# Performance work log

Hardware: AMD Instinct MI355X
Metric: run time of the kernel (lower is better)

## Reference

```python
import jax, jax.numpy as jnp
import numpy as np

B, N, C, H = 16, 577, 768, 12
D = C // H
BETA = 1.0
KEEP_RATIO = 0.5


def setup_inputs() -> dict:
    key = jax.random.key(0)
    k0, k1, k2, k3 = jax.random.split(key, 4)
    x = jax.random.normal(k0, (B, N, C), dtype=jnp.float32)
    # UCB visit-count buffer, strictly positive as accumulated counts would be
    ucb_count_score = jax.random.uniform(k1, (H, N), dtype=jnp.float32) * 50.0 + 1.0
    Wqkv = jax.random.normal(k2, (3 * C, C), dtype=jnp.float32) * 0.02
    Wproj = jax.random.normal(k3, (C, C), dtype=jnp.float32) * 0.02
    bproj = jnp.zeros((C,), dtype=jnp.float32)
    counter = 60  # > 50 so pruning path is taken
    return {"x": x, "ucb_count_score": ucb_count_score, "Wqkv": Wqkv,
            "Wproj": Wproj, "bproj": bproj, "counter": counter}


def reference(x, ucb_count_score, Wqkv, Wproj, bproj, counter):
    # UCBAttention.forward with pruning_enabled=True, selection_mode='ucb',
    # ucb_update_enabled=True, exclude_cls=True, dropout=0 (eval).
    Bs, Ns, Cs = x.shape
    scale = D ** -0.5
    k_keep = max(1, int((Ns - 1) * KEEP_RATIO))  # _get_k with keep_ratio

    qkv = (x @ Wqkv.T).reshape(Bs, Ns, 3, H, D).transpose(2, 0, 3, 1, 4)  # [3,B,H,N,D]
    q, k, v = qkv[0], qkv[1], qkv[2]
    attn_scores = jnp.einsum('bhqd,bhkd->bhqk', q, k) * scale
    attn_probs = jax.nn.softmax(attn_scores, axis=-1)  # [B,H,N,N]

    # UCB scores over patches (CLS excluded)
    patch_scores = attn_probs[:, :, :, 1:].mean(axis=2)            # [B,H,N-1]
    expl = BETA * jnp.sqrt(jnp.log(counter + 1.0) / (ucb_count_score[:, 1:] + 1e-6))
    ucb_scores = patch_scores + expl[None, :, :]                   # [B,H,N-1]
    global_ucb = ucb_scores.mean(axis=1)                           # [B,N-1]
    _, topk_rel = jax.lax.top_k(global_ucb, k_keep)                # [B,k]
    kept = topk_rel + 1                                            # token indices

    # keep-vector: CLS (0) always kept; mask[i,j] = kept[i] OR kept[j]
    kv_mask = (jnp.zeros((Bs, Ns), attn_probs.dtype)
               .at[jnp.arange(Bs)[:, None], kept].set(1.0)
               .at[:, 0].set(1.0))                                 # [B,N]
    mask = jnp.maximum(kv_mask[:, None, :, None], kv_mask[:, None, None, :])  # [B,1,N,N]

    pruned = attn_probs * mask
    pruned = pruned / (pruned.sum(axis=-1, keepdims=True) + 1e-8)
    context = jnp.einsum('bhqk,bhkd->bhqd', pruned, v)             # [B,H,N,D]

    out = context.transpose(0, 2, 1, 3).reshape(Bs, Ns, Cs) @ Wproj.T + bproj

    # score_delta: +1/B at each kept token column, broadcast over heads
    delta = jnp.zeros((Ns,), jnp.float32).at[kept.reshape(-1)].add(1.0 / Bs)
    score_delta = jnp.broadcast_to(delta[None, :], ucb_count_score.shape)
    return out, score_delta, kept
```

## Files before the change

### kernel.cpp

```cpp
#include <hip/hip_runtime.h>
#include <cstdio>
#include <cstdint>

#define B_    16
#define N_    577
#define C_    768
#define H_    12
#define D_    64
#define KKEEP 288
#define SCALE 0.125f
#define LOG2E 1.4426950408889634f
#define M_TOT (B_ * N_)
#define NKT   24
#define PLROW ((size_t)N_ * 64)

typedef __bf16 bf16x8_t __attribute__((ext_vector_type(8)));
typedef __bf16 bf16x4_t __attribute__((ext_vector_type(4)));
typedef float  f32x4_t  __attribute__((ext_vector_type(4)));
typedef unsigned int u32x4_t __attribute__((ext_vector_type(4)));
typedef unsigned int u32x2_t __attribute__((ext_vector_type(2)));

__device__ __forceinline__ f32x4_t mfma_bf16(bf16x8_t a, bf16x8_t b, f32x4_t c) {
    return __builtin_amdgcn_mfma_f32_16x16x32_bf16(a, b, c, 0, 0, 0);
}

__device__ __forceinline__ void gload16(const ushort* g, ushort* l) {
    __builtin_amdgcn_global_load_lds(
        (const __attribute__((address_space(1))) void*)g,
        (__attribute__((address_space(3))) void*)l, 16, 0, 0);
}
#define VMCNT(n) asm volatile("s_waitcnt vmcnt(" #n ")" ::: "memory")
#define LGKM0()  asm volatile("s_waitcnt lgkmcnt(0)" ::: "memory")
#define SB() __builtin_amdgcn_sched_barrier(0)

__device__ __forceinline__ int xcd_swz(int bid, int nwg) {
    int q = nwg >> 3, r = nwg & 7;
    int xcd = bid & 7, off = bid >> 3;
    int base = (xcd < r) ? xcd * (q + 1) : r * (q + 1) + (xcd - r) * q;
    return base + off;
}

__device__ __forceinline__ void splitf(float x, unsigned int &hi, unsigned int &lo) {
    unsigned int u = __float_as_uint(x);
    hi = u >> 16;
    float r = x - __uint_as_float(u & 0xffff0000u);
    lo = __float_as_uint(r) >> 16;
}
__device__ __forceinline__ unsigned int bf16rne(float x) {
    unsigned int u = __float_as_uint(x);
    return (u + 0x7fffu + ((u >> 16) & 1u)) >> 16;
}

__device__ __forceinline__ void pack_tile(const float* __restrict__ src,
                                          ushort* __restrict__ dH,
                                          ushort* __restrict__ dL,
                                          int nrows, int tile) {
    int kt = tile % NKT, mt = tile / NKT;
    int w = threadIdx.x;
    int row = w >> 1, h = w & 1;
    int m = mt * 128 + row;
    int sw = (row >> 1) & 3;
    float f[16];
    if (m < nrows) {
        const float* s = src + (size_t)m * C_ + kt * 32;
        int sa = (2 * h) ^ sw, sb = (2 * h + 1) ^ sw;
        *(float4*)&f[0]  = *(const float4*)(s + sa * 8);
        *(float4*)&f[4]  = *(const float4*)(s + sa * 8 + 4);
        *(float4*)&f[8]  = *(const float4*)(s + sb * 8);
        *(float4*)&f[12] = *(const float4*)(s + sb * 8 + 4);
    } else {
#pragma unroll
        for (int i = 0; i < 16; i++) f[i] = 0.f;
    }
    unsigned hi[16], lo[16];
#pragma unroll
    for (int i = 0; i < 16; i++) splitf(f[i], hi[i], lo[i]);
    u32x4_t h0 = {hi[0] | (hi[1] << 16), hi[2] | (hi[3] << 16),
                  hi[4] | (hi[5] << 16), hi[6] | (hi[7] << 16)};
    u32x4_t h1 = {hi[8] | (hi[9] << 16), hi[10] | (hi[11] << 16),
                  hi[12] | (hi[13] << 16), hi[14] | (hi[15] << 16)};
    u32x4_t l0 = {lo[0] | (lo[1] << 16), lo[2] | (lo[3] << 16),
                  lo[4] | (lo[5] << 16), lo[6] | (lo[7] << 16)};
    u32x4_t l1 = {lo[8] | (lo[9] << 16), lo[10] | (lo[11] << 16),
                  lo[12] | (lo[13] << 16), lo[14] | (lo[15] << 16)};
    size_t dbase = (size_t)tile * 4096 + row * 32;
    *(u32x4_t*)&dH[dbase + (2 * h) * 8]     = h0;
    *(u32x4_t*)&dH[dbase + (2 * h + 1) * 8] = h1;
    *(u32x4_t*)&dL[dbase + (2 * h) * 8]     = l0;
    *(u32x4_t*)&dL[dbase + (2 * h + 1) * 8] = l1;
}

__device__ __forceinline__ void pack_tile_rne(const float* __restrict__ src,
                                              ushort* __restrict__ dst,
                                              int nrows, int tile) {
    int kt = tile % NKT, mt = tile / NKT;
    int w = threadIdx.x;
    int row = w >> 1, h = w & 1;
    int m = mt * 128 + row;
    int sw = (row >> 1) & 3;
    float f[16];
    if (m < nrows) {
        const float* s = src + (size_t)m * C_ + kt * 32;
        int sa = (2 * h) ^ sw, sb = (2 * h + 1) ^ sw;
        *(float4*)&f[0]  = *(const float4*)(s + sa * 8);
        *(float4*)&f[4]  = *(const float4*)(s + sa * 8 + 4);
        *(float4*)&f[8]  = *(const float4*)(s + sb * 8);
        *(float4*)&f[12] = *(const float4*)(s + sb * 8 + 4);
    } else {
#pragma unroll
        for (int i = 0; i < 16; i++) f[i] = 0.f;
    }
    unsigned hi[16];
#pragma unroll
    for (int i = 0; i < 16; i++) hi[i] = bf16rne(f[i]);
    u32x4_t h0 = {hi[0] | (hi[1] << 16), hi[2] | (hi[3] << 16),
                  hi[4] | (hi[5] << 16), hi[6] | (hi[7] << 16)};
    u32x4_t h1 = {hi[8] | (hi[9] << 16), hi[10] | (hi[11] << 16),
                  hi[12] | (hi[13] << 16), hi[14] | (hi[15] << 16)};
    size_t dbase = (size_t)tile * 4096 + row * 32;
    *(u32x4_t*)&dst[dbase + (2 * h) * 8]     = h0;
    *(u32x4_t*)&dst[dbase + (2 * h + 1) * 8] = h1;
}

#define NXP 1752
#define NWP 432
#define NPJ 144
#define NZ  37

__global__ __launch_bounds__(256) void pack_all_kernel(const float* __restrict__ x,
                                                       const float* __restrict__ Wqkv,
                                                       const float* __restrict__ Wproj,
                                                       ushort* __restrict__ XplH,
                                                       ushort* __restrict__ XplL,
                                                       ushort* __restrict__ WplH,
                                                       ushort* __restrict__ WplL,
                                                       ushort* __restrict__ Wpjb,
                                                       float* __restrict__ kvmask) {
    int bid = blockIdx.x;
    if (bid < NXP) {
        pack_tile(x, XplH, XplL, M_TOT, bid);
    } else if (bid < NXP + NWP) {
        pack_tile(Wqkv, WplH, WplL, 3 * C_, bid - NXP);
    } else if (bid < NXP + NWP + NPJ) {
        pack_tile_rne(Wproj, Wpjb, C_, bid - NXP - NWP);
    } else {
        int i = (bid - NXP - NWP - NPJ) * 256 + threadIdx.x;
        if (i < B_ * N_) kvmask[i] = 0.f;
    }
}

__device__ __forceinline__ bf16x8_t fragT(const ushort* H, int row, int c, int ls) {
    int phys = ((c << 2) + ls) ^ (row & 7);
    return __builtin_bit_cast(bf16x8_t, *(const u32x4_t*)&H[(row << 6) + (phys << 3)]);
}

__global__ __launch_bounds__(256) void gemm_qkv_mfma(const ushort* __restrict__ XplH,
                                                     const ushort* __restrict__ XplL,
                                                     const ushort* __restrict__ WplH,
                                                     const ushort* __restrict__ WplL,
                                                     ushort* __restrict__ qhp,
                                                     ushort* __restrict__ qlp,
                                                     ushort* __restrict__ khp,
                                                     ushort* __restrict__ klp,
                                                     ushort* __restrict__ vtp) {
    __shared__ ushort SMEM[24576];
    ushort* Ah = SMEM;
    ushort* Al = SMEM + 8192;
    ushort* Bh = SMEM + 16384;
    ushort* Bl = SMEM + 20480;
    const int bid = xcd_swz(blockIdx.x, 18 * 73);
    const int bx = bid % 18, by = bid / 18;
    const int tid = threadIdx.x;
    const int lane = tid & 63, wave = tid >> 6;
    const int wr = wave >> 1, wc = wave & 1;
    const int lr = lane & 15, ls = lane >> 4;
    const int m0 = by * 128;
    const int o0 = wave * 1024, o1 = o0 + 512;
    const int la = lane * 8;
    const size_t abase = (size_t)by * NKT * 4096;
    const size_t bbase = (size_t)bx * NKT * 4096;
    f32x4_t acc[4][4] = {};

    if (bx < 12) {
        auto stageA = [&](int buf, int kt) {
            const size_t ta = abase + (size_t)kt * 4096;
            gload16(XplH + ta + o0 + la, &Ah[buf * 4096 + o0]);
            gload16(XplH + ta + o1 + la, &Ah[buf * 4096 + o1]);
            gload16(XplL + ta + o0 + la, &Al[buf * 4096 + o0]);
            gload16(XplL + ta + o1 + la, &Al[buf * 4096 + o1]);
        };
        auto stageB = [&](int kt) {
            const size_t tb = bbase + (size_t)kt * 4096;
            gload16(WplH + tb + o0 + la, &Bh[o0]);
            gload16(WplH + tb + o1 + la, &Bh[o1]);
            gload16(WplL + tb + o0 + la, &Bl[o0]);
            gload16(WplL + tb + o1 + la, &Bl[o1]);
        };
        stageA(0, 0);
        stageB(0);
        VMCNT(0);
        SB(); __builtin_amdgcn_s_barrier(); SB();
#pragma unroll 1
        for (int kt = 0; kt < NKT; ++kt) {
            const int cur = kt & 1;
            if (kt + 1 < NKT) stageA(cur ^ 1, kt + 1);
            bf16x8_t fah[4], fal[4], fbh[4], fbl[4];
#pragma unroll
            for (int i = 0; i < 4; i++) {
                int rowA = wr * 64 + i * 16 + lr;
                int pa = ls ^ ((rowA >> 1) & 3);
                fah[i] = __builtin_bit_cast(bf16x8_t, *(const u32x4_t*)&Ah[cur * 4096 + rowA * 32 + pa * 8]);
                fal[i] = __builtin_bit_cast(bf16x8_t, *(const u32x4_t*)&Al[cur * 4096 + rowA * 32 + pa * 8]);
                int rowB = wc * 64 + i * 16 + lr;
                int pb = ls ^ ((rowB >> 1) & 3);
                fbh[i] = __builtin_bit_cast(bf16x8_t, *(const u32x4_t*)&Bh[rowB * 32 + pb * 8]);
                fbl[i] = __builtin_bit_cast(bf16x8_t, *(const u32x4_t*)&Bl[rowB * 32 + pb * 8]);
            }
            LGKM0(); SB();
            __builtin_amdgcn_s_barrier();
            SB();
            if (kt + 1 < NKT) stageB(kt + 1);
            __builtin_amdgcn_s_setprio(1);
#pragma unroll
            for (int i = 0; i < 4; i++)
#pragma unroll
                for (int j = 0; j < 4; j++) {
                    acc[i][j] = mfma_bf16(fah[i], fbh[j], acc[i][j]);
                    acc[i][j] = mfma_bf16(fah[i], fbl[j], acc[i][j]);
                    acc[i][j] = mfma_bf16(fal[i], fbh[j], acc[i][j]);
                }
            __builtin_amdgcn_s_setprio(0);
            if (kt + 1 < NKT) {
                VMCNT(0); SB();
                __builtin_amdgcn_s_barrier();
                SB();
            }
        }
        const int n0 = bx * 128;
        const int s = n0 / C_;
        __syncthreads();
        unsigned* T = (unsigned*)SMEM;
        const float sc = (s == 0) ? SCALE * LOG2E : 1.0f;
        ushort* dh = (s == 1) ? khp : qhp;
        ushort* dl = (s == 1) ? klp : qlp;
        const int hh0 = (n0 % C_) / D_;
#pragma unroll 1
        for (int round = 0; round < 2; ++round) {
            if (wr == round) {
#pragma unroll
                for (int j = 0; j < 4; j++) {
                    int nl = wc * 64 + j * 16 + lr;
#pragma unroll
                    for (int i = 0; i < 4; i++) {
#pragma unroll
                        for (int r = 0; r < 4; r++) {
                            int ml = wr * 64 + i * 16 + ls * 4 + r;
                            unsigned hi, lo;
                            splitf(acc[i][j][r] * sc, hi, lo);
                            int idx = (ml & 63) * 128 +
                                      ((((nl >> 3) ^ ((ml >> 2) & 7)) << 3) | (nl & 7));
                            T[idx] = hi | (lo << 16);
                        }
                    }
                }
            }
            __syncthreads();
#pragma unroll
            for (int it = 0; it < 4; ++it) {
                int g = it * 256 + tid;
                int sl = g & 7;
                int m_local64 = (g >> 3) & 63;
                int hh_half = g >> 9;
                int m_local = round * 64 + m_local64;
                int m = m0 + m_local;
                if (m < M_TOT) {
                    int b = m / N_, n = m % N_;
                    int dg = sl ^ (n & 7);
                    int grp = (hh_half * 8 + dg) ^ ((m_local >> 2) & 7);
                    const unsigned* src = &T[m_local64 * 128 + grp * 8];
                    u32x4_t a = *(const u32x4_t*)src;
                    u32x4_t bvv = *(const u32x4_t*)(src + 4);
                    u32x4_t hiv = {(a[0] & 0xffffu) | (a[1] << 16),
                                   (a[2] & 0xffffu) | (a[3] << 16),
                                   (bvv[0] & 0xffffu) | (bvv[1] << 16),
                                   (bvv[2] & 0xffffu) | (bvv[3] << 16)};
                    u32x4_t lov = {(a[0] >> 16) | (a[1] & 0xffff0000u),
                                   (a[2] >> 16) | (a[3] & 0xffff0000u),
                                   (bvv[0] >> 16) | (bvv[1] & 0xffff0000u),
                                   (bvv[2] >> 16) | (bvv[3] & 0xffff0000u)};
                    size_t off = (size_t)(b * H_ + hh0 + hh_half) * PLROW + (size_t)n * 64 + sl * 8;
                    *(u32x4_t*)&dh[off] = hiv;
                    *(u32x4_t*)&dl[off] = lov;
                }
            }
            if (round == 0) __syncthreads();
        }
    } else {
        auto stageA = [&](int buf, int kt) {
            const size_t ta = abase + (size_t)kt * 4096;
            gload16(XplH + ta + o0 + la, &Ah[buf * 4096 + o0]);
            gload16(XplH + ta + o1 + la, &Ah[buf * 4096 + o1]);
            gload16(XplL + ta + o0 + la, &Al[buf * 4096 + o0]);
            gload16(XplL + ta + o1 + la, &Al[buf * 4096 + o1]);
        };
        auto stageB = [&](int kt) {
            const size_t tb = bbase + (size_t)kt * 4096;
            gload16(WplH + tb + o0 + la, &Bh[o0]);
            gload16(WplH + tb + o1 + la, &Bh[o1]);
        };
        stageA(0, 0);
        stageB(0);
        VMCNT(0);
        SB(); __builtin_amdgcn_s_barrier(); SB();
#pragma unroll 1
        for (int kt = 0; kt < NKT; ++kt) {
            const int cur = kt & 1;
            if (kt + 1 < NKT) stageA(cur ^ 1, kt + 1);
            bf16x8_t fah[4], fal[4], fbh[4];
#pragma unroll
            for (int i = 0; i < 4; i++) {
                int rowA = wr * 64 + i * 16 + lr;
                int pa = ls ^ ((rowA >> 1) & 3);
                fah[i] = __builtin_bit_cast(bf16x8_t, *(const u32x4_t*)&Ah[cur * 4096 + rowA * 32 + pa * 8]);
                fal[i] = __builtin_bit_cast(bf16x8_t, *(const u32x4_t*)&Al[cur * 4096 + rowA * 32 + pa * 8]);
                int rowB = wc * 64 + i * 16 + lr;
                int pb = ls ^ ((rowB >> 1) & 3);
                fbh[i] = __builtin_bit_cast(bf16x8_t, *(const u32x4_t*)&Bh[rowB * 32 + pb * 8]);
            }
            LGKM0(); SB();
            __builtin_amdgcn_s_barrier();
            SB();
            if (kt + 1 < NKT) stageB(kt + 1);
            __builtin_amdgcn_s_setprio(1);
#pragma unroll
            for (int i = 0; i < 4; i++)
#pragma unroll
                for (int j = 0; j < 4; j++) {
                    acc[i][j] = mfma_bf16(fah[i], fbh[j], acc[i][j]);
                    acc[i][j] = mfma_bf16(fal[i], fbh[j], acc[i][j]);
                }
            __builtin_amdgcn_s_setprio(0);
            if (kt + 1 < NKT) {
                VMCNT(0); SB();
                __builtin_amdgcn_s_barrier();
                SB();
            }
        }
        const int n0v = (bx - 12) * 128;
#pragma unroll
        for (int j = 0; j < 4; j++) {
            int ng = n0v + wc * 64 + j * 16 + lr;
            int hh = ng / D_;
            int d = ng % D_;
#pragma unroll
            for (int i = 0; i < 4; i++) {
                int mg0 = m0 + wr * 64 + i * 16 + ls * 4;
#pragma unroll
                for (int r = 0; r < 4; r++) {
                    int m = mg0 + r;
                    if (m < M_TOT) {
                        int b = m / N_, n = m % N_;
                        int jt = n >> 6, jl = n & 63;
                        size_t off = ((size_t)(b * H_ + hh) * 10 + jt) * 4096 +
                                     (size_t)d * 64 + (((jl >> 3) ^ (d & 7)) << 3) + (jl & 7);
                        vtp[off] = __builtin_bit_cast(unsigned short, (__bf16)acc[i][j][r]);
                    }
                }
            }
        }
    }
}

__global__ __launch_bounds__(512) void attn_rowsum_mfma(const ushort* __restrict__ qh,
                                                        const ushort* __restrict__ ql,
                                                        const ushort* __restrict__ kh,
                                                        const ushort* __restrict__ kl,
                                                        float* __restrict__ w) {
    __shared__ ushort Qh[8192], Ql[8192];
    __shared__ ushort Kh[4096], Kl[4096];
    __shared__ float red[8][64];
    const int bid = xcd_swz(blockIdx.x, 5 * B_ * H_);
    const int bh = bid / 5, q0 = (bid % 5) * 128;
    const int tid = threadIdx.x, lane = tid & 63, wv = tid >> 6;
    const int wg = wv >> 2, wl = wv & 3;
    const int lr = lane & 15, ls = lane >> 4;
    const size_t bho = (size_t)bh * PLROW;
    const ushort* qhp = qh + bho; const ushort* qlp = ql + bho;
    const ushort* khp = kh + bho; const ushort* klp = kl + bho;
    auto qrow = [&](int rr) { return (size_t)min(q0 + wv * 16 + rr * 8 + (lane >> 3), N_ - 1) * 64 + (lane & 7) * 8; };
    gload16(qhp + qrow(0), &Qh[wv * 1024]);
    gload16(qhp + qrow(1), &Qh[wv * 1024 + 512]);
    gload16(qlp + qrow(0), &Ql[wv * 1024]);
    gload16(qlp + qrow(1), &Ql[wv * 1024 + 512]);
    auto krow = [&](int j0) { return (size_t)min(j0 + wv * 8 + (lane >> 3), N_ - 1) * 64 + (lane & 7) * 8; };
    auto stageK = [&](int j0) {
        gload16(khp + krow(j0), &Kh[wv * 512]);
        gload16(klp + krow(j0), &Kl[wv * 512]);
    };
    stageK(0);
    VMCNT(0);
    __syncthreads();
    bf16x8_t fqh[4][2], fql[4][2];
#pragma unroll
    for (int i = 0; i < 4; i++)
#pragma unroll
        for (int c = 0; c < 2; c++) {
            fqh[i][c] = fragT(Qh, wg * 64 + i * 16 + lr, c, ls);
            fql[i][c] = fragT(Ql, wg * 64 + i * 16 + lr, c, ls);
        }
    float rs[4] = {0.f, 0.f, 0.f, 0.f};
#pragma unroll 1
    for (int t = 0; t < 10; ++t) {
        bf16x8_t fkh[2], fkl[2];
#pragma unroll
        for (int c = 0; c < 2; c++) {
            fkh[c] = fragT(Kh, wl * 16 + lr, c, ls);
            fkl[c] = fragT(Kl, wl * 16 + lr, c, ls);
        }
        LGKM0(); SB();
        __builtin_amdgcn_s_barrier();
        SB();
        if (t < 9) stageK((t + 1) * 64);
        int jbase = t * 64 + wl * 16 + ls * 4;
#pragma unroll
        for (int i = 0; i < 4; i++) {
            f32x4_t s = {0.f, 0.f, 0.f, 0.f};
            __builtin_amdgcn_s_setprio(1);
#pragma unroll
            for (int c = 0; c < 2; c++) {
                s = mfma_bf16(fkh[c], fqh[i][c], s);
                s = mfma_bf16(fkh[c], fql[i][c], s);
                s = mfma_bf16(fkl[c], fqh[i][c], s);
            }
            __builtin_amdgcn_s_setprio(0);
#pragma unroll
            for (int r = 0; r < 4; r++)
                rs[i] += (jbase + r < N_) ? __builtin_amdgcn_exp2f(s[r]) : 0.f;
        }
        if (t < 9) {
            VMCNT(0); SB();
            __builtin_amdgcn_s_barrier();
            SB();
        }
    }
#pragma unroll
    for (int i = 0; i < 4; i++) {
        float v2 = rs[i];
        v2 += __shfl_xor(v2, 16);
        v2 += __shfl_xor(v2, 32);
        if (ls == 0) red[wv][i * 16 + lr] = v2;
    }
    __syncthreads();
    if (tid < 128) {
        int grp = tid >> 6, qlc = tid & 63;
        float s = red[grp * 4 + 0][qlc] + red[grp * 4 + 1][qlc] +
                  red[grp * 4 + 2][qlc] + red[grp * 4 + 3][qlc];
        int qn = q0 + tid;
        if (qn < N_) w[(size_t)bh * N_ + qn] = 1.0f / s;
    }
}

__global__ __launch_bounds__(512) void attn_colsum_mfma(const ushort* __restrict__ qh,
                                                        const ushort* __restrict__ ql,
                                                        const ushort* __restrict__ kh,
                                                        const ushort* __restrict__ kl,
                                                        const float* __restrict__ w,
                                                        float* __restrict__ colsum) {
    __shared__ ushort KhS[8192], KlS[8192];
    __shared__ ushort Qh[4096], Ql[4096];
    __shared__ float wsAll[640];
    __shared__ float red[8][64];
    const int bid = xcd_swz(blockIdx.x, 5 * B_ * H_);
    const int bh = bid / 5, j0 = (bid % 5) * 128;
    const int tid = threadIdx.x, lane = tid & 63, wv = tid >> 6;
    const int wg = wv >> 2, wl = wv & 3;
    const int lr = lane & 15, ls = lane >> 4;
    const size_t bho = (size_t)bh * PLROW;
    const ushort* qhp = qh + bho; const ushort* qlp = ql + bho;
    const ushort* khp = kh + bho; const ushort* klp = kl + bho;
    auto krow = [&](int rr) { return (size_t)min(j0 + wv * 16 + rr * 8 + (lane >> 3), N_ - 1) * 64 + (lane & 7) * 8; };
    gload16(khp + krow(0), &KhS[wv * 1024]);
    gload16(khp + krow(1), &KhS[wv * 1024 + 512]);
    gload16(klp + krow(0), &KlS[wv * 1024]);
    gload16(klp + krow(1), &KlS[wv * 1024 + 512]);
    auto qrow2 = [&](int qt) { return (size_t)min(qt + wv * 8 + (lane >> 3), N_ - 1) * 64 + (lane & 7) * 8; };
    auto stageQ = [&](int qt) {
        gload16(qhp + qrow2(qt), &Qh[wv * 512]);
        gload16(qlp + qrow2(qt), &Ql[wv * 512]);
    };
    stageQ(0);
    for (int i2 = tid; i2 < 640; i2 += 512)
        wsAll[i2] = (i2 < N_) ? w[(size_t)bh * N_ + i2] : 0.f;
    VMCNT(0);
    __syncthreads();
    bf16x8_t fkh[4][2], fkl[4][2];
#pragma unroll
    for (int i = 0; i < 4; i++)
#pragma unroll
        for (int c = 0; c < 2; c++) {
            fkh[i][c] = fragT(KhS, wg * 64 + i * 16 + lr, c, ls);
            fkl[i][c] = fragT(KlS, wg * 64 + i * 16 + lr, c, ls);
        }
    float cs[4] = {0.f, 0.f, 0.f, 0.f};
#pragma unroll 1
    for (int t = 0; t < 10; ++t) {
        bf16x8_t fqh[2], fql[2];
#pragma unroll
        for (int c = 0; c < 2; c++) {
            fqh[c] = fragT(Qh, wl * 16 + lr, c, ls);
            fql[c] = fragT(Ql, wl * 16 + lr, c, ls);
        }
        float wq[4];
#pragma unroll
        for (int r = 0; r < 4; r++) wq[r] = wsAll[t * 64 + wl * 16 + ls * 4 + r];
        LGKM0(); SB();
        __builtin_amdgcn_s_barrier();
        SB();
        if (t < 9) stageQ((t + 1) * 64);
#pragma unroll
        for (int i = 0; i < 4; i++) {
            f32x4_t s = {0.f, 0.f, 0.f, 0.f};
            __builtin_amdgcn_s_setprio(1);
#pragma unroll
            for (int c = 0; c < 2; c++) {
                s = mfma_bf16(fqh[c], fkh[i][c], s);
                s = mfma_bf16(fql[c], fkh[i][c], s);
                s = mfma_bf16(fqh[c], fkl[i][c], s);
            }
            __builtin_amdgcn_s_setprio(0);
#pragma unroll
            for (int r = 0; r < 4; r++) cs[i] += __builtin_amdgcn_exp2f(s[r]) * wq[r];
        }
        if (t < 9) {
            VMCNT(0); SB();
            __builtin_amdgcn_s_barrier();
            SB();
        }
    }
#pragma unroll
    for (int i = 0; i < 4; i++) {
        float v2 = cs[i];
        v2 += __shfl_xor(v2, 16);
        v2 += __shfl_xor(v2, 32);
        if (ls == 0) red[wv][i * 16 + lr] = v2;
    }
    __syncthreads();
    if (tid < 128) {
        int grp = tid >> 6, jlc = tid & 63;
        float t2 = red[grp * 4 + 0][jlc] + red[grp * 4 + 1][jlc] +
                   red[grp * 4 + 2][jlc] + red[grp * 4 + 3][jlc];
        int jn = j0 + tid;
        if (jn < N_) colsum[(size_t)bh * N_ + jn] = t2;
    }
}

__global__ __launch_bounds__(512) void topk_kernel(const float* __restrict__ colsum,
                                                   const float* __restrict__ ucb_count,
                                                   const int* __restrict__ counter,
                                                   float* __restrict__ kept_out,
                                                   float* __restrict__ kvmask) {
    __shared__ float sv[1024];
    __shared__ int si[1024];
    int b = blockIdx.x, tid = threadIdx.x;
    float lc = logf((float)counter[0] + 1.0f);
    for (int t = tid; t < 1024; t += 512) {
        if (t < N_ - 1) {
            int tok = t + 1;
            float accv = 0.f;
#pragma unroll
            for (int h = 0; h < H_; h++) {
                float csv = colsum[(size_t)(b * H_ + h) * N_ + tok];
                float patch = csv * (1.0f / (float)N_);
                float cnt = ucb_count[h * N_ + tok];
                float expl = sqrtf(lc / (cnt + 1e-6f));
                accv += patch + expl;
            }
            sv[t] = accv * (1.0f / (float)H_);
            si[t] = t;
        } else {
            sv[t] = -INFINITY;
            si[t] = 1 << 20;
        }
    }
    __syncthreads();
    for (int kk = 2; kk <= 1024; kk <<= 1) {
        for (int jj = kk >> 1; jj > 0; jj >>= 1) {
            for (int t = tid; t < 1024; t += 512) {
                int ixj = t ^ jj;
                if (ixj > t) {
                    float v1 = sv[t], v2 = sv[ixj];
                    int i1 = si[t], i2 = si[ixj];
                    bool before21 = (v2 > v1) || (v2 == v1 && i2 < i1);
                    bool dirDesc = ((t & kk) == 0);
                    if (before21 == dirDesc) {
                        sv[t] = v2; sv[ixj] = v1;
                        si[t] = i2; si[ixj] = i1;
                    }
                }
            }
            __syncthreads();
        }
    }
    for (int r = tid; r < KKEEP; r += 512) {
        int tok = si[r] + 1;
        kept_out[b * KKEEP + r] = (float)tok;
        kvmask[b * N_ + tok] = 1.0f;
    }
    if (tid == 0) kvmask[b * N_] = 1.0f;
}

__global__ __launch_bounds__(512) void attn_ctx_mfma(const ushort* __restrict__ qh,
                                                     const ushort* __restrict__ ql,
                                                     const ushort* __restrict__ kh,
                                                     const ushort* __restrict__ vtp,
                                                     const float* __restrict__ kvmask,
                                                     ushort* __restrict__ ctxb,
                                                     float* __restrict__ sd) {
    if (blockIdx.x >= 5 * B_ * H_) {
        int idx = (blockIdx.x - 5 * B_ * H_) * 512 + threadIdx.x;
        if (idx < H_ * N_) {
            int n = idx % N_;
            float d = 0.f;
            if (n != 0) {
#pragma unroll
                for (int b = 0; b < B_; b++) d += kvmask[b * N_ + n];
            }
            sd[idx] = d * (1.0f / (float)B_);
        }
        return;
    }
    __shared__ ushort Kh[4096], Vt[4096];
    __shared__ ushort Pl[2][4096];
    __shared__ float mkAll[640];
    float (*red)[64] = (float(*)[64])&Pl[0][0];
    float* inv = (float*)&Pl[1][0];
    const int bid = xcd_swz(blockIdx.x, 5 * B_ * H_);
    const int bh = bid / 5, q0 = (bid % 5) * 128;
    const int b = bh / H_, h = bh % H_;
    const int tid = threadIdx.x, lane = tid & 63, wv = tid >> 6;
    const int wg = wv >> 2, wl = wv & 3;
    const int lr = lane & 15, ls = lane >> 4;
    const size_t bho = (size_t)bh * PLROW;
    const ushort* qhp = qh + bho; const ushort* qlp = ql + bho;
    const ushort* khp = kh + bho;
    const ushort* vtb = vtp + (size_t)bh * 10 * 4096;
    ushort* PlS = &Pl[0][0];
    for (int i2 = tid; i2 < 640; i2 += 512)
        mkAll[i2] = (i2 < N_) ? kvmask[(size_t)b * N_ + i2] : 0.f;
    auto qrow = [&](int rr) { return (size_t)min(q0 + wv * 16 + rr * 8 + (lane >> 3), N_ - 1) * 64 + (lane & 7) * 8; };
    bf16x8_t fqh[4][2], fql[4][2];
    gload16(qhp + qrow(0), &PlS[wv * 1024]);
    gload16(qhp + qrow(1), &PlS[wv * 1024 + 512]);
    VMCNT(0); __syncthreads();
#pragma unroll
    for (int i = 0; i < 4; i++)
#pragma unroll
        for (int c = 0; c < 2; c++)
            fqh[i][c] = fragT(PlS, wg * 64 + i * 16 + lr, c, ls);
    __syncthreads();
    gload16(qlp + qrow(0), &PlS[wv * 1024]);
    gload16(qlp + qrow(1), &PlS[wv * 1024 + 512]);
    VMCNT(0); __syncthreads();
#pragma unroll
    for (int i = 0; i < 4; i++)
#pragma unroll
        for (int c = 0; c < 2; c++)
            fql[i][c] = fragT(PlS, wg * 64 + i * 16 + lr, c, ls);
    __syncthreads();
    auto krow = [&](int j0) { return (size_t)min(j0 + wv * 8 + (lane >> 3), N_ - 1) * 64 + (lane & 7) * 8; };
    auto stageKV = [&](int t) {
        gload16(khp + krow(t * 64), &Kh[wv * 512]);
        gload16(vtb + (size_t)t * 4096 + wv * 512 + lane * 8, &Vt[wv * 512]);
    };
    float mq[4];
#pragma unroll
    for (int i = 0; i < 4; i++) mq[i] = mkAll[q0 + wg * 64 + i * 16 + lr];
    stageKV(0);
    VMCNT(0);
    SB(); __builtin_amdgcn_s_barrier(); SB();
    f32x4_t acc[4] = {};
    float psums[4] = {0.f, 0.f, 0.f, 0.f};
#pragma unroll 1
    for (int t = 0; t < 10; ++t) {
        bf16x8_t fkh[2], fv[2];
#pragma unroll
        for (int c = 0; c < 2; c++) {
            fkh[c] = fragT(Kh, wl * 16 + lr, c, ls);
            fv[c]  = fragT(Vt, wl * 16 + lr, c, ls);
        }
        LGKM0(); SB();
        __builtin_amdgcn_s_barrier();
        SB();
        if (t < 9) stageKV(t + 1);
        int jloc = wl * 16 + ls * 4;
        float jmv[4], jbias[4];
#pragma unroll
        for (int r = 0; r < 4; r++) {
            int j = t * 64 + jloc + r;
            jmv[r] = mkAll[t * 64 + jloc + r];
            jbias[r] = (j < N_) ? 0.f : -16384.f;
        }
#pragma unroll
        for (int i = 0; i < 4; i++) {
            f32x4_t s = {0.f, 0.f, 0.f, 0.f};
            __builtin_amdgcn_s_setprio(1);
#pragma unroll
            for (int c = 0; c < 2; c++) {
                s = mfma_bf16(fkh[c], fqh[i][c], s);
                s = mfma_bf16(fkh[c], fql[i][c], s);
            }
            __builtin_amdgcn_s_setprio(0);
            bf16x4_t pb;
            float mqi = mq[i];
#pragma unroll
            for (int r = 0; r < 4; r++) {
                float p = __builtin_amdgcn_exp2f(s[r] + jbias[r]) * fmaxf(mqi, jmv[r]);
                psums[i] += p;
                pb[r] = (__bf16)p;
            }
            int row = i * 16 + lr;
            int slot = ((wl << 1) + (ls >> 1)) ^ (row & 7);
            *(u32x2_t*)&Pl[wg][(row << 6) + (slot << 3) + ((ls & 1) << 2)] =
                __builtin_bit_cast(u32x2_t, pb);
        }
        SB(); LGKM0(); SB();
        __builtin_amdgcn_s_barrier();
        SB();
        __builtin_amdgcn_s_setprio(1);
#pragma unroll
        for (int i = 0; i < 4; i++) {
            bf16x8_t fp0 = fragT(Pl[wg], i * 16 + lr, 0, ls);
            bf16x8_t fp1 = fragT(Pl[wg], i * 16 + lr, 1, ls);
            acc[i] = mfma_bf16(fv[0], fp0, acc[i]);
            acc[i] = mfma_bf16(fv[1], fp1, acc[i]);
        }
        __builtin_amdgcn_s_setprio(0);
        if (t < 9) {
            VMCNT(0); SB();
            __builtin_amdgcn_s_barrier();
            SB();
        }
    }
    __syncthreads();
#pragma unroll
    for (int i = 0; i < 4; i++) {
        float v2 = psums[i];
        v2 += __shfl_xor(v2, 16);
        v2 += __shfl_xor(v2, 32);
        if (ls == 0) red[wv][i * 16 + lr] = v2;
    }
    __syncthreads();
    if (tid < 128) {
        int grp = tid >> 6, qlc = tid & 63;
        float t2 = red[grp * 4 + 0][qlc] + red[grp * 4 + 1][qlc] +
                   red[grp * 4 + 2][qlc] + red[grp * 4 + 3][qlc];
        inv[tid] = 1.0f / (t2 + 1e-8f);
    }
    __syncthreads();
#pragma unroll
    for (int i = 0; i < 4; i++) {
        int qn = q0 + wg * 64 + i * 16 + lr;
        if (qn < N_) {
            float rn = inv[wg * 64 + i * 16 + lr];
            bf16x4_t ov;
            ov[0] = (__bf16)(acc[i][0] * rn);
            ov[1] = (__bf16)(acc[i][1] * rn);
            ov[2] = (__bf16)(acc[i][2] * rn);
            ov[3] = (__bf16)(acc[i][3] * rn);
            int m = b * N_ + qn;
            int col = h * D_ + wl * 16 + ls * 4;
            int mt = m >> 7, rowl = m & 127;
            int kt2 = col >> 5, c32 = col & 31;
            int phys = (c32 >> 3) ^ ((rowl >> 1) & 3);
            size_t off = ((size_t)(mt * NKT + kt2)) * 4096 + rowl * 32 + phys * 8 + (c32 & 7);
            *(u32x2_t*)&ctxb[off] = __builtin_bit_cast(u32x2_t, ov);
        }
    }
}

__global__ __launch_bounds__(256) void gemm_proj_mfma(const ushort* __restrict__ Apl,
                                                      const ushort* __restrict__ Bpl,
                                                      const float* __restrict__ bias,
                                                      float* __restrict__ out) {
    __shared__ ushort Ab[2][4096], Bb[2][4096];
    const int bid = xcd_swz(blockIdx.x, 6 * 73);
    const int bx = bid % 6, by = bid / 6;
    const int tid = threadIdx.x;
    const int lane = tid & 63, wave = tid >> 6;
    const int wr = wave >> 1, wc = wave & 1;
    const int lr = lane & 15, ls = lane >> 4;
    const int m0 = by * 128, n0 = bx * 128;
    const int o0 = wave * 1024, o1 = o0 + 512;
    const int la = lane * 8;
    const size_t abase = (size_t)by * NKT * 4096;
    const size_t bbase = (size_t)bx * NKT * 4096;
    f32x4_t acc[4][4] = {};

    auto stage = [&](int buf, int kt) {
        const size_t ta = abase + (size_t)kt * 4096;
        const size_t tb = bbase + (size_t)kt * 4096;
        gload16(Apl + ta + o0 + la, &Ab[buf][o0]);
        gload16(Apl + ta + o1 + la, &Ab[buf][o1]);
        gload16(Bpl + tb + o0 + la, &Bb[buf][o0]);
        gload16(Bpl + tb + o1 + la, &Bb[buf][o1]);
    };
    stage(0, 0);
#pragma unroll 1
    for (int kt = 0; kt < NKT; ++kt) {
        const int cur = kt & 1;
        if (kt + 1 < NKT) {
            stage(cur ^ 1, kt + 1);
            VMCNT(4);
        } else {
            VMCNT(0);
        }
        SB();
        __builtin_amdgcn_s_barrier();
        SB();
        bf16x8_t fa[4], fb[4];
#pragma unroll
        for (int i = 0; i < 4; i++) {
            int rowA = wr * 64 + i * 16 + lr;
            int pa = ls ^ ((rowA >> 1) & 3);
            fa[i] = __builtin_bit_cast(bf16x8_t, *(const u32x4_t*)&Ab[cur][rowA * 32 + pa * 8]);
            int rowB = wc * 64 + i * 16 + lr;
            int pb = ls ^ ((rowB >> 1) & 3);
            fb[i] = __builtin_bit_cast(bf16x8_t, *(const u32x4_t*)&Bb[cur][rowB * 32 + pb * 8]);
        }
#pragma unroll
        for (int i = 0; i < 4; i++)
#pragma unroll
            for (int j = 0; j < 4; j++)
                acc[i][j] = mfma_bf16(fa[i], fb[j], acc[i][j]);
        if (kt + 1 < NKT) {
            SB();
            __builtin_amdgcn_s_barrier();
        }
    }
#pragma unroll
    for (int j = 0; j < 4; j++) {
        int ng = n0 + wc * 64 + j * 16 + lr;
        float bb = bias[ng];
#pragma unroll
        for (int i = 0; i < 4; i++) {
            int mg0 = m0 + wr * 64 + i * 16 + ls * 4;
#pragma unroll
            for (int r = 0; r < 4; r++) {
                int m = mg0 + r;
                if (m < M_TOT) out[(size_t)m * C_ + ng] = acc[i][j][r] + bb;
            }
        }
    }
}

extern "C" void kernel_launch(void* const* d_in, const int* in_sizes, int n_in,
                              void* d_out, int out_size, void* d_ws, size_t ws_size,
                              hipStream_t stream) {
    const float* x     = (const float*)d_in[0];
    const float* ucb   = (const float*)d_in[1];
    const float* Wqkv  = (const float*)d_in[2];
    const float* Wproj = (const float*)d_in[3];
    const float* bproj = (const float*)d_in[4];
    const int*   counter = (const int*)d_in[5];

    const size_t BHN  = (size_t)B_ * H_ * N_;
    const size_t XPL  = (size_t)(73 * 128) * C_;
    const size_t WPL  = (size_t)3 * C_ * C_;
    const size_t WPJ  = (size_t)C_ * C_;
    const size_t PLN  = (size_t)192 * PLROW;
    const size_t VTSZ = (size_t)192 * 10 * 4096;

    ushort* qhp  = (ushort*)d_ws;
    ushort* qlp  = qhp + PLN;
    ushort* khp  = qlp + PLN;
    ushort* klp  = khp + PLN;
    ushort* vtp  = klp + PLN;
    ushort* XplH = vtp + VTSZ;
    ushort* XplL = XplH + XPL;
    ushort* ctxb = XplH;
    ushort* WplH = XplL + XPL;
    ushort* WplL = WplH + WPL;
    ushort* Wpjb = WplL + WPL;
    float*  w    = (float*)(Wpjb + WPJ);
    float*  colsum = w + BHN;
    float*  kvmask = colsum + BHN;
    size_t need = ((char*)(kvmask + (size_t)B_ * N_)) - (char*)d_ws;
    if (ws_size < need) {
        fprintf(stderr, "kernel_launch: ws too small, need %zu have %zu\n",
                need, ws_size);
        return;
    }

    float* out  = (float*)d_out;
    float* sd   = out + (size_t)B_ * N_ * C_;
    float* kept = sd + (size_t)H_ * N_;

    pack_all_kernel<<<NXP + NWP + NPJ + NZ, 256, 0, stream>>>(
        x, Wqkv, Wproj, XplH, XplL, WplH, WplL, Wpjb, kvmask);

    gemm_qkv_mfma<<<18 * 73, 256, 0, stream>>>(XplH, XplL, WplH, WplL,
                                               qhp, qlp, khp, klp, vtp);
    attn_rowsum_mfma<<<5 * B_ * H_, 512, 0, stream>>>(qhp, qlp, khp, klp, w);
    attn_colsum_mfma<<<5 * B_ * H_, 512, 0, stream>>>(qhp, qlp, khp, klp, w, colsum);
    topk_kernel<<<B_, 512, 0, stream>>>(colsum, ucb, counter, kept, kvmask);
    attn_ctx_mfma<<<5 * B_ * H_ + 14, 512, 0, stream>>>(qhp, qlp, khp, vtp,
                                                        kvmask, ctxb, sd);
    gemm_proj_mfma<<<6 * 73, 256, 0, stream>>>(ctxb, Wpjb, bproj, out);
}
```

Before: 271.1 us.

## Fuse attention row-sum and column-sum passes into one kernel with partial colsums

The separate row-normalizer and column-sum attention kernels are merged. Each block first computes the softmax row sums for its 128 query rows. It then sweeps K again in the same launch, reusing the Q fragments already in registers, and writes per-query-tile partial column sums, which the top-k kernel adds up across the 5 tiles. This removes one kernel launch and one reload of Q/K, at the cost of a second QK^T pass inside the block, extra barriers and shuffles per tile, and a 5x larger partial colsum buffer.

```diff
diff --git a/kernel.cpp b/kernel.cpp
--- a/kernel.cpp
+++ b/kernel.cpp
@@ -371,16 +371,18 @@
     }
 }
 
-__global__ __launch_bounds__(512) void attn_rowsum_mfma(const ushort* __restrict__ qh,
-                                                        const ushort* __restrict__ ql,
-                                                        const ushort* __restrict__ kh,
-                                                        const ushort* __restrict__ kl,
-                                                        float* __restrict__ w) {
+__global__ __launch_bounds__(512) void attn_rc_mfma(const ushort* __restrict__ qh,
+                                                    const ushort* __restrict__ ql,
+                                                    const ushort* __restrict__ kh,
+                                                    const ushort* __restrict__ kl,
+                                                    float* __restrict__ colsum_part) {
     __shared__ ushort Qh[8192], Ql[8192];
     __shared__ ushort Kh[4096], Kl[4096];
     __shared__ float red[8][64];
+    __shared__ float wsld[128];
+    __shared__ float cpart[2][64];
     const int bid = xcd_swz(blockIdx.x, 5 * B_ * H_);
-    const int bh = bid / 5, q0 = (bid % 5) * 128;
+    const int bh = bid / 5, qt5 = bid % 5, q0 = qt5 * 128;
     const int tid = threadIdx.x, lane = tid & 63, wv = tid >> 6;
     const int wg = wv >> 2, wl = wv & 3;
     const int lr = lane & 15, ls = lane >> 4;
@@ -455,81 +457,59 @@
         int grp = tid >> 6, qlc = tid & 63;
         float s = red[grp * 4 + 0][qlc] + red[grp * 4 + 1][qlc] +
                   red[grp * 4 + 2][qlc] + red[grp * 4 + 3][qlc];
-        int qn = q0 + tid;
-        if (qn < N_) w[(size_t)bh * N_ + qn] = 1.0f / s;
-    }
-}
-
-__global__ __launch_bounds__(512) void attn_colsum_mfma(const ushort* __restrict__ qh,
-                                                        const ushort* __restrict__ ql,
-                                                        const ushort* __restrict__ kh,
-                                                        const ushort* __restrict__ kl,
-                                                        const float* __restrict__ w,
-                                                        float* __restrict__ colsum) {
-    __shared__ ushort KhS[8192], KlS[8192];
-    __shared__ ushort Qh[4096], Ql[4096];
-    __shared__ float wsAll[640];
-    __shared__ float red[8][64];
-    const int bid = xcd_swz(blockIdx.x, 5 * B_ * H_);
-    const int bh = bid / 5, j0 = (bid % 5) * 128;
-    const int tid = threadIdx.x, lane = tid & 63, wv = tid >> 6;
-    const int wg = wv >> 2, wl = wv & 3;
-    const int lr = lane & 15, ls = lane >> 4;
-    const size_t bho = (size_t)bh * PLROW;
-    const ushort* qhp = qh + bho; const ushort* qlp = ql + bho;
-    const ushort* khp = kh + bho; const ushort* klp = kl + bho;
-    auto krow = [&](int rr) { return (size_t)min(j0 + wv * 16 + rr * 8 + (lane >> 3), N_ - 1) * 64 + (lane & 7) * 8; };
-    gload16(khp + krow(0), &KhS[wv * 1024]);
-    gload16(khp + krow(1), &KhS[wv * 1024 + 512]);
-    gload16(klp + krow(0), &KlS[wv * 1024]);
-    gload16(klp + krow(1), &KlS[wv * 1024 + 512]);
-    auto qrow2 = [&](int qt) { return (size_t)min(qt + wv * 8 + (lane >> 3), N_ - 1) * 64 + (lane & 7) * 8; };
-    auto stageQ = [&](int qt) {
-        gload16(qhp + qrow2(qt), &Qh[wv * 512]);
-        gload16(qlp + qrow2(qt), &Ql[wv * 512]);
-    };
-    stageQ(0);
-    for (int i2 = tid; i2 < 640; i2 += 512)
-        wsAll[i2] = (i2 < N_) ? w[(size_t)bh * N_ + i2] : 0.f;
+        wsld[grp * 64 + qlc] = (q0 + grp * 64 + qlc < N_) ? 1.0f / s : 0.f;
+    }
+    __syncthreads();
+    float wq[4];
+#pragma unroll
+    for (int i = 0; i < 4; i++) wq[i] = wsld[wg * 64 + i * 16 + lr];
+    stageK(0);
     VMCNT(0);
-    __syncthreads();
-    bf16x8_t fkh[4][2], fkl[4][2];
-#pragma unroll
-    for (int i = 0; i < 4; i++)
-#pragma unroll
-        for (int c = 0; c < 2; c++) {
-            fkh[i][c] = fragT(KhS, wg * 64 + i * 16 + lr, c, ls);
-            fkl[i][c] = fragT(KlS, wg * 64 + i * 16 + lr, c, ls);
-        }
-    float cs[4] = {0.f, 0.f, 0.f, 0.f};
+    SB(); __builtin_amdgcn_s_barrier(); SB();
+    float* cpout = colsum_part + ((size_t)qt5 * (B_ * H_) + bh) * N_;
 #pragma unroll 1
     for (int t = 0; t < 10; ++t) {
-        bf16x8_t fqh[2], fql[2];
+        bf16x8_t fkh[2], fkl[2];
 #pragma unroll
         for (int c = 0; c < 2; c++) {
-            fqh[c] = fragT(Qh, wl * 16 + lr, c, ls);
-            fql[c] = fragT(Ql, wl * 16 + lr, c, ls);
-        }
-        float wq[4];
-#pragma unroll
-        for (int r = 0; r < 4; r++) wq[r] = wsAll[t * 64 + wl * 16 + ls * 4 + r];
+            fkh[c] = fragT(Kh, wl * 16 + lr, c, ls);
+            fkl[c] = fragT(Kl, wl * 16 + lr, c, ls);
+        }
         LGKM0(); SB();
         __builtin_amdgcn_s_barrier();
         SB();
-        if (t < 9) stageQ((t + 1) * 64);
+        if (t < 9) stageK((t + 1) * 64);
+        float cj[4] = {0.f, 0.f, 0.f, 0.f};
 #pragma unroll
         for (int i = 0; i < 4; i++) {
             f32x4_t s = {0.f, 0.f, 0.f, 0.f};
             __builtin_amdgcn_s_setprio(1);
 #pragma unroll
             for (int c = 0; c < 2; c++) {
-                s = mfma_bf16(fqh[c], fkh[i][c], s);
-                s = mfma_bf16(fql[c], fkh[i][c], s);
-                s = mfma_bf16(fqh[c], fkl[i][c], s);
+                s = mfma_bf16(fkh[c], fqh[i][c], s);
+                s = mfma_bf16(fkh[c], fql[i][c], s);
+                s = mfma_bf16(fkl[c], fqh[i][c], s);
             }
             __builtin_amdgcn_s_setprio(0);
 #pragma unroll
-            for (int r = 0; r < 4; r++) cs[i] += __builtin_amdgcn_exp2f(s[r]) * wq[r];
+            for (int r = 0; r < 4; r++)
+                cj[r] += __builtin_amdgcn_exp2f(s[r]) * wq[i];
+        }
+#pragma unroll
+        for (int r = 0; r < 4; r++) {
+            float v2 = cj[r];
+            v2 += __shfl_xor(v2, 1);
+            v2 += __shfl_xor(v2, 2);
+            v2 += __shfl_xor(v2, 4);
+            v2 += __shfl_xor(v2, 8);
+            if (lr == 0) cpart[wg][wl * 16 + ls * 4 + r] = v2;
+        }
+        LGKM0(); SB();
+        __builtin_amdgcn_s_barrier();
+        SB();
+        if (tid < 64) {
+            int j = t * 64 + tid;
+            if (j < N_) cpout[j] = cpart[0][tid] + cpart[1][tid];
         }
         if (t < 9) {
             VMCNT(0); SB();
@@ -537,24 +517,9 @@
             SB();
         }
     }
-#pragma unroll
-    for (int i = 0; i < 4; i++) {
-        float v2 = cs[i];
-        v2 += __shfl_xor(v2, 16);
-        v2 += __shfl_xor(v2, 32);
-        if (ls == 0) red[wv][i * 16 + lr] = v2;
-    }
-    __syncthreads();
-    if (tid < 128) {
-        int grp = tid >> 6, jlc = tid & 63;
-        float t2 = red[grp * 4 + 0][jlc] + red[grp * 4 + 1][jlc] +
-                   red[grp * 4 + 2][jlc] + red[grp * 4 + 3][jlc];
-        int jn = j0 + tid;
-        if (jn < N_) colsum[(size_t)bh * N_ + jn] = t2;
-    }
-}
-
-__global__ __launch_bounds__(512) void topk_kernel(const float* __restrict__ colsum,
+}
+
+__global__ __launch_bounds__(512) void topk_kernel(const float* __restrict__ colsum_part,
                                                    const float* __restrict__ ucb_count,
                                                    const int* __restrict__ counter,
                                                    float* __restrict__ kept_out,
@@ -563,13 +528,18 @@
     __shared__ int si[1024];
     int b = blockIdx.x, tid = threadIdx.x;
     float lc = logf((float)counter[0] + 1.0f);
+    const size_t QSTRIDE = (size_t)(B_ * H_) * N_;
     for (int t = tid; t < 1024; t += 512) {
         if (t < N_ - 1) {
             int tok = t + 1;
             float accv = 0.f;
 #pragma unroll
             for (int h = 0; h < H_; h++) {
-                float csv = colsum[(size_t)(b * H_ + h) * N_ + tok];
+                size_t base = (size_t)(b * H_ + h) * N_ + tok;
+                float csv = 0.f;
+#pragma unroll
+                for (int qt = 0; qt < 5; qt++)
+                    csv += colsum_part[qt * QSTRIDE + base];
                 float patch = csv * (1.0f / (float)N_);
                 float cnt = ucb_count[h * N_ + tok];
                 float expl = sqrtf(lc / (cnt + 1e-6f));
@@ -881,9 +851,8 @@
     ushort* WplH = XplL + XPL;
     ushort* WplL = WplH + WPL;
     ushort* Wpjb = WplL + WPL;
-    float*  w    = (float*)(Wpjb + WPJ);
-    float*  colsum = w + BHN;
-    float*  kvmask = colsum + BHN;
+    float*  colsum_part = (float*)(Wpjb + WPJ);
+    float*  kvmask = colsum_part + 5 * BHN;
     size_t need = ((char*)(kvmask + (size_t)B_ * N_)) - (char*)d_ws;
     if (ws_size < need) {
         fprintf(stderr, "kernel_launch: ws too small, need %zu have %zu\n",
@@ -900,9 +869,8 @@
 
     gemm_qkv_mfma<<<18 * 73, 256, 0, stream>>>(XplH, XplL, WplH, WplL,
                                                qhp, qlp, khp, klp, vtp);
-    attn_rowsum_mfma<<<5 * B_ * H_, 512, 0, stream>>>(qhp, qlp, khp, klp, w);
-    attn_colsum_mfma<<<5 * B_ * H_, 512, 0, stream>>>(qhp, qlp, khp, klp, w, colsum);
-    topk_kernel<<<B_, 512, 0, stream>>>(colsum, ucb, counter, kept, kvmask);
+    attn_rc_mfma<<<5 * B_ * H_, 512, 0, stream>>>(qhp, qlp, khp, klp, colsum_part);
+    topk_kernel<<<B_, 512, 0, stream>>>(colsum_part, ucb, counter, kept, kvmask);
     attn_ctx_mfma<<<5 * B_ * H_ + 14, 512, 0, stream>>>(qhp, qlp, khp, vtp,
                                                         kvmask, ctxb, sd);
     gemm_proj_mfma<<<6 * 73, 256, 0, stream>>>(ctxb, Wpjb, bproj, out);
```

After: 277.6 us. 1.02x slower.
